# Performance work log

Hardware: AMD Instinct MI355X
Metric: run time of the kernel (lower is better)

The kernel has to match this reference:

```python
import jax, jax.numpy as jnp
import numpy as np

B, T, D = 4, 2048, 1024
H = 16
DH = D // H

def setup_inputs() -> dict:
    key = jax.random.key(0)
    k1, k2, k3 = jax.random.split(key, 3)
    x = jax.random.normal(k1, (B, T, D), dtype=jnp.float32)
    causal_mask = jnp.tril(jnp.ones((T, T), dtype=bool))[None, None]  # (1,1,T,T)
    Wqkv = jax.random.normal(k2, (D, 3 * D), dtype=jnp.float32) * (1.0 / np.sqrt(D))
    Wout = jax.random.normal(k3, (D, D), dtype=jnp.float32) * (1.0 / np.sqrt(D))
    return {"x": x, "causal_mask": causal_mask, "Wqkv": Wqkv, "Wout": Wout}

def reference(x, causal_mask, Wqkv, Wout):
    Bb, Tt, C = x.shape
    scale = jnp.sqrt(jnp.asarray(DH, dtype=x.dtype))
    qkv = x @ Wqkv                                   # (B,T,3D)
    qkv = qkv.reshape(Bb, Tt, 3, H, DH)
    qkv = jnp.transpose(qkv, (2, 0, 3, 1, 4))        # (3,B,H,T,DH)
    q, k, v = qkv[0], qkv[1], qkv[2]
    attn = jnp.einsum('bhqd,bhkd->bhqk', q, k) / scale
    attn = jnp.where(causal_mask, attn, jnp.asarray(-jnp.inf, dtype=attn.dtype))
    attn = jax.nn.softmax(attn, axis=-1)             # dropout p=0 -> identity
    out = jnp.einsum('bhqk,bhkd->bhqd', attn, v)     # (B,H,T,DH)
    out = jnp.transpose(out, (0, 2, 1, 3)).reshape(Bb, Tt, C)
    return out @ Wout
```

## Files before the change

### kernel.cpp

```cpp
#include <hip/hip_runtime.h>
#include <hip/hip_bf16.h>
#include <math.h>


#define Bb 4
#define Tt 2048
#define Dd 1024
#define Hh 16
#define DH 64
#define Mrows (Bb*Tt)
#define NEGBIG (-1.0e30f)
#define KB64 (Dd/64)
#define CHUNKS 1024
#define TILEU16 8192

typedef unsigned short u16;
typedef __attribute__((ext_vector_type(8))) short bf16x8;
typedef __attribute__((ext_vector_type(4))) float f32x4;
typedef __attribute__((ext_vector_type(4))) unsigned int u32x4;

__device__ __forceinline__ u16 f2bf(float f) {
    union { float f; unsigned int i; } v; v.f = f;
    unsigned int x = v.i;
    return (u16)((x + 0x7fffu + ((x >> 16) & 1u)) >> 16);
}

__device__ __forceinline__ unsigned int cvt_pk_bf16(float lo, float hi) {
    unsigned int r;
    asm("v_cvt_pk_bf16_f32 %0, %1, %2" : "=v"(r) : "v"(lo), "v"(hi));
    return r;
}

__device__ __forceinline__ void perm32swap(unsigned& x, unsigned& y) {
    asm("v_permlane32_swap_b32 %0, %1" : "+v"(x), "+v"(y));
}
__device__ __forceinline__ void perm16swap(unsigned& x, unsigned& y) {
    asm("v_permlane16_swap_b32 %0, %1" : "+v"(x), "+v"(y));
}

__device__ __forceinline__ float exp2_(float x) {
#if __has_builtin(__builtin_amdgcn_exp2f)
    return __builtin_amdgcn_exp2f(x);
#else
    return __expf(x * 0.69314718056f);
#endif
}

typedef __attribute__((address_space(1))) const void glob_cv;
typedef __attribute__((address_space(3))) void lds_v;
__device__ __forceinline__ void gl2lds16(const void* g, void* l) {
    __builtin_amdgcn_global_load_lds((glob_cv*)g, (lds_v*)l, 16, 0, 0);
}

__global__ __launch_bounds__(256) void convert_x_tiled(const float* __restrict__ src,
                                                       u16* __restrict__ dst) {
    const int mb = blockIdx.x >> 4, kb = blockIdx.x & 15;
    const int row = threadIdx.x & 127, half = threadIdx.x >> 7;
    const float* s = src + (size_t)(mb * 128 + row) * Dd + kb * 64 + half * 32;
    u16* base = dst + (size_t)blockIdx.x * TILEU16;
    #pragma unroll
    for (int cq = 0; cq < 4; ++cq) {
        const int kq = half * 4 + cq;
        float4 f0 = *(const float4*)(s + cq * 8);
        float4 f1 = *(const float4*)(s + cq * 8 + 4);
        uint4 o;
        o.x = cvt_pk_bf16(f0.x, f0.y); o.y = cvt_pk_bf16(f0.z, f0.w);
        o.z = cvt_pk_bf16(f1.x, f1.y); o.w = cvt_pk_bf16(f1.z, f1.w);
        *(uint4*)(base + (size_t)(kq * 128 + row) * 8) = o;
    }
}

__global__ __launch_bounds__(256) void convert_w_tiled(const float* __restrict__ W,
                                                       u16* __restrict__ Wt,
                                                       int N) {
    __shared__ u16 t[128][68];
    const int nb = blockIdx.x, kb = blockIdx.y;
    const int k0 = kb * 64, n0 = nb * 128;
    const int k = threadIdx.x >> 2, ng = threadIdx.x & 3;
    const float* s = W + (size_t)(k0 + k) * N + n0 + ng * 32;
    #pragma unroll
    for (int i = 0; i < 8; ++i) {
        float4 f = *(const float4*)(s + i * 4);
        const int n = ng * 32 + i * 4;
        t[n + 0][k] = f2bf(f.x); t[n + 1][k] = f2bf(f.y);
        t[n + 2][k] = f2bf(f.z); t[n + 3][k] = f2bf(f.w);
    }
    __syncthreads();
    u16* base = Wt + (size_t)(nb * KB64 + kb) * TILEU16;
    #pragma unroll
    for (int it = 0; it < 4; ++it) {
        const int c = it * 256 + threadIdx.x;
        const int row = c & 127, kq = c >> 7;
        union { u16 u[8]; uint4 v; } o;
        #pragma unroll
        for (int j = 0; j < 8; ++j) o.u[j] = t[row][kq * 8 + j];
        *(uint4*)(base + (size_t)c * 8) = o.v;
    }
}

template <int MODE>
__global__ __launch_bounds__(256) void gemm_mfma(const u16* __restrict__ At,
                                                 const u16* __restrict__ Bt,
                                                 u16* __restrict__ Qo,
                                                 u16* __restrict__ KT,
                                                 u16* __restrict__ VtT,
                                                 float* __restrict__ Out) {
    __shared__ u16 As[8 * 128 * 8];
    __shared__ u16 Bs[8 * 128 * 8];
    const int tid  = threadIdx.x;
    const int lane = tid & 63, w = tid >> 6;
    const int ml   = lane & 15, q = lane >> 4;
    const int wm   = w >> 1, wn = w & 1;
    const int m0 = blockIdx.y * 128;

    const u16* Abase = At + (size_t)blockIdx.y * KB64 * TILEU16;
    const u16* Bbase = Bt + (size_t)blockIdx.x * KB64 * TILEU16;

    f32x4 acc[4][4];
    #pragma unroll
    for (int i = 0; i < 4; ++i)
        #pragma unroll
        for (int j = 0; j < 4; ++j) acc[i][j] = (f32x4){0.f, 0.f, 0.f, 0.f};

    for (int kb = 0; kb < KB64; ++kb) {
        __syncthreads();
        const u16* Ak = Abase + (size_t)kb * TILEU16;
        const u16* Bk = Bbase + (size_t)kb * TILEU16;
        #pragma unroll
        for (int it = 0; it < 4; ++it) {
            const int c = it * 256 + tid;
            gl2lds16(Ak + (size_t)c * 8, (char*)As + c * 16);
            gl2lds16(Bk + (size_t)c * 8, (char*)Bs + c * 16);
        }
        __syncthreads();

        #pragma unroll
        for (int ks = 0; ks < 2; ++ks) {
            const int kq = ks * 4 + q;
            bf16x8 af[4], bfr[4];
            #pragma unroll
            for (int i = 0; i < 4; ++i)
                af[i] = *(const bf16x8*)((const char*)As +
                        ((kq * 128) + wm * 64 + i * 16 + ml) * 16);
            #pragma unroll
            for (int j = 0; j < 4; ++j)
                bfr[j] = *(const bf16x8*)((const char*)Bs +
                        ((kq * 128) + wn * 64 + j * 16 + ml) * 16);
            #pragma unroll
            for (int i = 0; i < 4; ++i)
                #pragma unroll
                for (int j = 0; j < 4; ++j)
                    acc[i][j] = __builtin_amdgcn_mfma_f32_16x16x32_bf16(
                            bfr[j], af[i], acc[i][j], 0, 0, 0);
        }
    }

    if (MODE == 0) {
        const int s  = (blockIdx.x * 128) >> 10;
        const int h0 = ((blockIdx.x * 128) & 1023) >> 6;
        #pragma unroll
        for (int i = 0; i < 4; ++i) {
            const int m  = m0 + wm * 64 + i * 16 + ml;
            const int bb = m >> 11, t = m & 2047;
            const int bhn = bb * Hh + h0 + wn;
            #pragma unroll
            for (int j = 0; j < 4; ++j) {
                const int dh = j * 16 + q * 4;
                if (s == 2) {
                    u16* vb = VtT + (size_t)(bhn * 16 + (t >> 7)) * TILEU16;
                    #pragma unroll
                    for (int r = 0; r < 4; ++r)
                        vb[(size_t)(((t >> 3) & 15) * 64 + dh + r) * 8 + (t & 7)]
                            = f2bf(acc[i][j][r]);
                } else if (s == 1) {
                    uint2 pk;
                    pk.x = cvt_pk_bf16(acc[i][j][0], acc[i][j][1]);
                    pk.y = cvt_pk_bf16(acc[i][j][2], acc[i][j][3]);
                    *(uint2*)(KT + (size_t)(bhn * 16 + (t >> 7)) * TILEU16 +
                              (size_t)((j * 2 + (q >> 1)) * 128 + (t & 127)) * 8 +
                              (q & 1) * 4) = pk;
                } else {
                    const float sc = 0.125f * 1.44269504089f;
                    uint2 pk;
                    pk.x = cvt_pk_bf16(acc[i][j][0] * sc, acc[i][j][1] * sc);
                    pk.y = cvt_pk_bf16(acc[i][j][2] * sc, acc[i][j][3] * sc);
                    *(uint2*)(Qo + ((size_t)bhn * Tt + t) * DH + dh) = pk;
                }
            }
        }
    } else {
        #pragma unroll
        for (int i = 0; i < 4; ++i) {
            const int m = m0 + wm * 64 + i * 16 + ml;
            #pragma unroll
            for (int j = 0; j < 4; ++j) {
                const int n = blockIdx.x * 128 + wn * 64 + j * 16 + q * 4;
                float4 st = {acc[i][j][0], acc[i][j][1], acc[i][j][2], acc[i][j][3]};
                *(float4*)(Out + (size_t)m * Dd + n) = st;
            }
        }
    }
}

__device__ __forceinline__ void softmax_pack(f32x4 (&st)[8], float& m_i, float& l_i,
                                             f32x4 (&accO)[4], unsigned (&d)[8],
                                             unsigned (&e)[8], int q, int qrow,
                                             bool diag) {
    if (diag) {
        #pragma unroll
        for (int kt = 0; kt < 8; ++kt)
            #pragma unroll
            for (int r = 0; r < 4; ++r)
                if (kt * 16 + q * 4 + r > qrow) st[kt][r] = NEGBIG;
    }
    float mx = NEGBIG;
    #pragma unroll
    for (int kt = 0; kt < 8; ++kt) {
        float a0 = fmaxf(st[kt][0], st[kt][1]);
        float a1 = fmaxf(st[kt][2], st[kt][3]);
        mx = fmaxf(fmaxf(mx, a0), a1);
    }
    mx = fmaxf(mx, __shfl_xor(mx, 16, 64));
    mx = fmaxf(mx, __shfl_xor(mx, 32, 64));

    float nm = m_i;
    if (__any(mx > m_i + 8.f)) {
        nm = fmaxf(m_i, mx);
        const float alpha = exp2_(m_i - nm);
        m_i = nm;
        l_i *= alpha;
        #pragma unroll
        for (int dt = 0; dt < 4; ++dt)
            #pragma unroll
            for (int r = 0; r < 4; ++r) accO[dt][r] *= alpha;
    }

    float rs = 0.f;
    #pragma unroll
    for (int kt = 0; kt < 8; ++kt) {
        const float p0 = exp2_(st[kt][0] - nm);
        const float p1 = exp2_(st[kt][1] - nm);
        const float p2 = exp2_(st[kt][2] - nm);
        const float p3 = exp2_(st[kt][3] - nm);
        rs += (p0 + p1) + (p2 + p3);
        d[kt] = cvt_pk_bf16(p0, p1);
        e[kt] = cvt_pk_bf16(p2, p3);
    }
    rs += __shfl_xor(rs, 16, 64);
    rs += __shfl_xor(rs, 32, 64);
    l_i += rs;
}

__device__ __forceinline__ bf16x8 build_bp(const unsigned (&d)[8],
                                           const unsigned (&e)[8], int s) {
    unsigned w0 = d[2 * s], w2 = d[2 * s + 1];
    perm32swap(w0, w2); perm16swap(w0, w2);
    unsigned w1 = e[2 * s], w3 = e[2 * s + 1];
    perm32swap(w1, w3); perm16swap(w1, w3);
    union { u32x4 u; bf16x8 b; } cv;
    cv.u = (u32x4){w0, w1, w2, w3};
    return cv.b;
}

__global__ __launch_bounds__(256, 3) void attn_mfma(const u16* __restrict__ Q,
                                                    const u16* __restrict__ KT,
                                                    const u16* __restrict__ VtT,
                                                    u16* __restrict__ AOT) {
    __shared__ u16 Ks[8 * 128 * 8];
    __shared__ u16 Vs[2][16 * 64 * 8];

    const int tid  = threadIdx.x;
    const int lane = tid & 63, w = tid >> 6;
    const int nl   = lane & 15, q = lane >> 4;
    const int bh = blockIdx.y, b = bh >> 4, h = bh & 15;
    const size_t kbase = (size_t)bh * Tt * DH;

    for (int phase = 0; phase < 2; ++phase) {
        const int qt = phase ? (15 - (int)blockIdx.x) : (int)blockIdx.x;
        const int q0 = qt * 128;
        const int nj = qt + 1;

        bf16x8 qf[2][2];
        #pragma unroll
        for (int qb = 0; qb < 2; ++qb)
            #pragma unroll
            for (int s = 0; s < 2; ++s)
                qf[qb][s] = *(const bf16x8*)(Q + kbase +
                        (size_t)(q0 + w * 32 + qb * 16 + nl) * DH + (s * 4 + q) * 8);

        float m_i[2] = {NEGBIG, NEGBIG};
        float l_i[2] = {0.f, 0.f};
        f32x4 accO[2][4];
        #pragma unroll
        for (int qb = 0; qb < 2; ++qb)
            #pragma unroll
            for (int dt = 0; dt < 4; ++dt) accO[qb][dt] = (f32x4){0.f, 0.f, 0.f, 0.f};

        __syncthreads();
        {
            const u16* Kb = KT  + (size_t)(bh * 16) * TILEU16;
            const u16* Vb = VtT + (size_t)(bh * 16) * TILEU16;
            #pragma unroll
            for (int it = 0; it < 4; ++it) {
                const int c = it * 256 + tid;
                gl2lds16(Kb + (size_t)c * 8, (char*)Ks + c * 16);
                gl2lds16(Vb + (size_t)c * 8, (char*)Vs[0] + c * 16);
            }
        }

        for (int jt = 0; jt < nj; ++jt) {
            const int buf = jt & 1;
            __syncthreads();

            f32x4 st0[8], st1[8];
            #pragma unroll
            for (int kt = 0; kt < 8; ++kt) {
                st0[kt] = (f32x4){0.f, 0.f, 0.f, 0.f};
                st1[kt] = (f32x4){0.f, 0.f, 0.f, 0.f};
            }
            __builtin_amdgcn_s_setprio(1);
            #pragma unroll
            for (int s = 0; s < 2; ++s) {
                #pragma unroll
                for (int kt = 0; kt < 8; ++kt) {
                    bf16x8 ak = *(const bf16x8*)((const char*)Ks +
                            ((s * 4 + q) * 128 + kt * 16 + nl) * 16);
                    st0[kt] = __builtin_amdgcn_mfma_f32_16x16x32_bf16(
                            ak, qf[0][s], st0[kt], 0, 0, 0);
                    st1[kt] = __builtin_amdgcn_mfma_f32_16x16x32_bf16(
                            ak, qf[1][s], st1[kt], 0, 0, 0);
                }
            }
            __builtin_amdgcn_s_setprio(0);

            __syncthreads();

            if (jt + 1 < nj) {
                const u16* Kb = KT  + (size_t)(bh * 16 + jt + 1) * TILEU16;
                const u16* Vb = VtT + (size_t)(bh * 16 + jt + 1) * TILEU16;
                #pragma unroll
                for (int it = 0; it < 4; ++it) {
                    const int c = it * 256 + tid;
                    gl2lds16(Kb + (size_t)c * 8, (char*)Ks + c * 16);
                    gl2lds16(Vb + (size_t)c * 8, (char*)Vs[buf ^ 1] + c * 16);
                }
            }

            const bool diag = (jt == nj - 1);
            unsigned d0[8], e0[8], d1[8], e1[8];
            softmax_pack(st0, m_i[0], l_i[0], accO[0], d0, e0, q, w * 32 + nl, diag);
            softmax_pack(st1, m_i[1], l_i[1], accO[1], d1, e1, q, w * 32 + 16 + nl, diag);

            __builtin_amdgcn_s_setprio(1);
            #pragma unroll
            for (int s = 0; s < 4; ++s) {
                bf16x8 bp0 = build_bp(d0, e0, s);
                bf16x8 bp1 = build_bp(d1, e1, s);
                #pragma unroll
                for (int dt = 0; dt < 4; ++dt) {
                    bf16x8 av = *(const bf16x8*)((const char*)Vs[buf] +
                            ((s * 4 + q) * 64 + dt * 16 + nl) * 16);
                    accO[0][dt] = __builtin_amdgcn_mfma_f32_16x16x32_bf16(
                            av, bp0, accO[0][dt], 0, 0, 0);
                    accO[1][dt] = __builtin_amdgcn_mfma_f32_16x16x32_bf16(
                            av, bp1, accO[1][dt], 0, 0, 0);
                }
            }
            __builtin_amdgcn_s_setprio(0);
        }

        #pragma unroll
        for (int qb = 0; qb < 2; ++qb) {
            const float inv = 1.0f / l_i[qb];
            const int t = q0 + w * 32 + qb * 16 + nl;
            const int m = b * Tt + t;
            u16* ab = AOT + (size_t)((m >> 7) * KB64 + h) * TILEU16;
            #pragma unroll
            for (int dt = 0; dt < 4; ++dt) {
                uint2 pk;
                pk.x = cvt_pk_bf16(accO[qb][dt][0] * inv, accO[qb][dt][1] * inv);
                pk.y = cvt_pk_bf16(accO[qb][dt][2] * inv, accO[qb][dt][3] * inv);
                *(uint2*)(ab + (size_t)((dt * 2 + (q >> 1)) * 128 + (m & 127)) * 8 +
                          (q & 1) * 4) = pk;
            }
        }
    }
}

extern "C" void kernel_launch(void* const* d_in, const int* in_sizes, int n_in,
                              void* d_out, int out_size, void* d_ws, size_t ws_size,
                              hipStream_t stream) {
    const float* x_raw    = (const float*)d_in[0];
    const float* Wqkv_raw = (const float*)d_in[2];
    const float* Wout_raw = (const float*)d_in[3];
    float* out = (float*)d_out;

    const size_t SZ = (size_t)Bb * Hh * Tt * DH;
    u16* ws = (u16*)d_ws;
    u16* Qw     = ws;
    u16* KT     = ws + SZ;
    u16* VtT    = ws + 2 * SZ;
    u16* AOT    = ws + 3 * SZ;
    u16* WqkvT  = ws + 4 * SZ;
    u16* WoutT  = WqkvT + (size_t)3 * Dd * Dd;
    u16* xT     = (u16*)d_out;

    convert_x_tiled<<<dim3(64 * KB64), 256, 0, stream>>>(x_raw, xT);
    convert_w_tiled<<<dim3(3 * Dd / 128, KB64), 256, 0, stream>>>(Wqkv_raw, WqkvT, 3 * Dd);
    convert_w_tiled<<<dim3(Dd / 128, KB64),     256, 0, stream>>>(Wout_raw, WoutT, Dd);

    gemm_mfma<0><<<dim3(3 * Dd / 128, Mrows / 128), 256, 0, stream>>>(xT, WqkvT, Qw, KT, VtT, nullptr);
    attn_mfma  <<<dim3(Tt / 256, Bb * Hh), 256, 0, stream>>>(Qw, KT, VtT, AOT);
    gemm_mfma<1><<<dim3(Dd / 128, Mrows / 128), 256, 0, stream>>>(AOT, WoutT, nullptr, nullptr, nullptr, out);
}
```

Baseline: 273.6 us.

## Fuse conversion kernels and read K/V fragments directly from global memory in attention

Merges the three fp32-to-bf16 conversion launches into one kernel that dispatches on block index, which removes two launches. The attention kernel also drops its LDS double-buffered K/V staging and the barriers around it, and loads MFMA operand fragments straight from global memory (relying on L1/L2), with launch bounds relaxed to allow more occupancy. This trades the synchronisation and LDS traffic for possibly higher global load latency and repeated loads of the same K/V tiles by each wave.

```diff
diff --git a/kernel.cpp b/kernel.cpp
--- a/kernel.cpp
+++ b/kernel.cpp
@@ -52,31 +52,12 @@
     __builtin_amdgcn_global_load_lds((glob_cv*)g, (lds_v*)l, 16, 0, 0);
 }
 
-__global__ __launch_bounds__(256) void convert_x_tiled(const float* __restrict__ src,
-                                                       u16* __restrict__ dst) {
-    const int mb = blockIdx.x >> 4, kb = blockIdx.x & 15;
-    const int row = threadIdx.x & 127, half = threadIdx.x >> 7;
-    const float* s = src + (size_t)(mb * 128 + row) * Dd + kb * 64 + half * 32;
-    u16* base = dst + (size_t)blockIdx.x * TILEU16;
-    #pragma unroll
-    for (int cq = 0; cq < 4; ++cq) {
-        const int kq = half * 4 + cq;
-        float4 f0 = *(const float4*)(s + cq * 8);
-        float4 f1 = *(const float4*)(s + cq * 8 + 4);
-        uint4 o;
-        o.x = cvt_pk_bf16(f0.x, f0.y); o.y = cvt_pk_bf16(f0.z, f0.w);
-        o.z = cvt_pk_bf16(f1.x, f1.y); o.w = cvt_pk_bf16(f1.z, f1.w);
-        *(uint4*)(base + (size_t)(kq * 128 + row) * 8) = o;
-    }
-}
-
-__global__ __launch_bounds__(256) void convert_w_tiled(const float* __restrict__ W,
-                                                       u16* __restrict__ Wt,
-                                                       int N) {
-    __shared__ u16 t[128][68];
-    const int nb = blockIdx.x, kb = blockIdx.y;
+__device__ __forceinline__ void conv_w_body(const float* __restrict__ W,
+                                            u16* __restrict__ Wt, int N,
+                                            int nb, int kb, int tid,
+                                            u16 (*t)[68]) {
     const int k0 = kb * 64, n0 = nb * 128;
-    const int k = threadIdx.x >> 2, ng = threadIdx.x & 3;
+    const int k = tid >> 2, ng = tid & 3;
     const float* s = W + (size_t)(k0 + k) * N + n0 + ng * 32;
     #pragma unroll
     for (int i = 0; i < 8; ++i) {
@@ -89,12 +70,44 @@
     u16* base = Wt + (size_t)(nb * KB64 + kb) * TILEU16;
     #pragma unroll
     for (int it = 0; it < 4; ++it) {
-        const int c = it * 256 + threadIdx.x;
+        const int c = it * 256 + tid;
         const int row = c & 127, kq = c >> 7;
         union { u16 u[8]; uint4 v; } o;
         #pragma unroll
         for (int j = 0; j < 8; ++j) o.u[j] = t[row][kq * 8 + j];
         *(uint4*)(base + (size_t)c * 8) = o.v;
+    }
+}
+
+__global__ __launch_bounds__(256) void convert_all(const float* __restrict__ x,
+                                                   const float* __restrict__ Wqkv,
+                                                   const float* __restrict__ Wout,
+                                                   u16* __restrict__ xT,
+                                                   u16* __restrict__ WqkvT,
+                                                   u16* __restrict__ WoutT) {
+    __shared__ u16 t[128][68];
+    const int bid = blockIdx.x, tid = threadIdx.x;
+    if (bid < 1024) {
+        const int mb = bid >> 4, kb = bid & 15;
+        const int row = tid & 127, half = tid >> 7;
+        const float* s = x + (size_t)(mb * 128 + row) * Dd + kb * 64 + half * 32;
+        u16* base = xT + (size_t)bid * TILEU16;
+        #pragma unroll
+        for (int cq = 0; cq < 4; ++cq) {
+            const int kq = half * 4 + cq;
+            float4 f0 = *(const float4*)(s + cq * 8);
+            float4 f1 = *(const float4*)(s + cq * 8 + 4);
+            uint4 o;
+            o.x = cvt_pk_bf16(f0.x, f0.y); o.y = cvt_pk_bf16(f0.z, f0.w);
+            o.z = cvt_pk_bf16(f1.x, f1.y); o.w = cvt_pk_bf16(f1.z, f1.w);
+            *(uint4*)(base + (size_t)(kq * 128 + row) * 8) = o;
+        }
+    } else if (bid < 1408) {
+        const int r = bid - 1024;
+        conv_w_body(Wqkv, WqkvT, 3 * Dd, r % 24, r / 24, tid, t);
+    } else {
+        const int r = bid - 1408;
+        conv_w_body(Wout, WoutT, Dd, r % 8, r / 8, tid, t);
     }
 }
 
@@ -262,13 +275,10 @@
     return cv.b;
 }
 
-__global__ __launch_bounds__(256, 3) void attn_mfma(const u16* __restrict__ Q,
-                                                    const u16* __restrict__ KT,
-                                                    const u16* __restrict__ VtT,
-                                                    u16* __restrict__ AOT) {
-    __shared__ u16 Ks[8 * 128 * 8];
-    __shared__ u16 Vs[2][16 * 64 * 8];
-
+__global__ __launch_bounds__(256) void attn_mfma(const u16* __restrict__ Q,
+                                                 const u16* __restrict__ KT,
+                                                 const u16* __restrict__ VtT,
+                                                 u16* __restrict__ AOT) {
     const int tid  = threadIdx.x;
     const int lane = tid & 63, w = tid >> 6;
     const int nl   = lane & 15, q = lane >> 4;
@@ -296,22 +306,10 @@
             #pragma unroll
             for (int dt = 0; dt < 4; ++dt) accO[qb][dt] = (f32x4){0.f, 0.f, 0.f, 0.f};
 
-        __syncthreads();
-        {
-            const u16* Kb = KT  + (size_t)(bh * 16) * TILEU16;
-            const u16* Vb = VtT + (size_t)(bh * 16) * TILEU16;
-            #pragma unroll
-            for (int it = 0; it < 4; ++it) {
-                const int c = it * 256 + tid;
-                gl2lds16(Kb + (size_t)c * 8, (char*)Ks + c * 16);
-                gl2lds16(Vb + (size_t)c * 8, (char*)Vs[0] + c * 16);
-            }
-        }
-
-        for (int jt = 0; jt < nj; ++jt) {
-            const int buf = jt & 1;
-            __syncthreads();
-
+        const u16* Kb = KT  + (size_t)(bh * 16) * TILEU16;
+        const u16* Vb = VtT + (size_t)(bh * 16) * TILEU16;
+
+        for (int jt = 0; jt < nj; ++jt, Kb += TILEU16, Vb += TILEU16) {
             f32x4 st0[8], st1[8];
             #pragma unroll
             for (int kt = 0; kt < 8; ++kt) {
@@ -323,8 +321,8 @@
             for (int s = 0; s < 2; ++s) {
                 #pragma unroll
                 for (int kt = 0; kt < 8; ++kt) {
-                    bf16x8 ak = *(const bf16x8*)((const char*)Ks +
-                            ((s * 4 + q) * 128 + kt * 16 + nl) * 16);
+                    bf16x8 ak = *(const bf16x8*)(Kb +
+                            (size_t)(((s * 4 + q) * 128 + kt * 16 + nl) * 8));
                     st0[kt] = __builtin_amdgcn_mfma_f32_16x16x32_bf16(
                             ak, qf[0][s], st0[kt], 0, 0, 0);
                     st1[kt] = __builtin_amdgcn_mfma_f32_16x16x32_bf16(
@@ -333,19 +331,6 @@
             }
             __builtin_amdgcn_s_setprio(0);
 
-            __syncthreads();
-
-            if (jt + 1 < nj) {
-                const u16* Kb = KT  + (size_t)(bh * 16 + jt + 1) * TILEU16;
-                const u16* Vb = VtT + (size_t)(bh * 16 + jt + 1) * TILEU16;
-                #pragma unroll
-                for (int it = 0; it < 4; ++it) {
-                    const int c = it * 256 + tid;
-                    gl2lds16(Kb + (size_t)c * 8, (char*)Ks + c * 16);
-                    gl2lds16(Vb + (size_t)c * 8, (char*)Vs[buf ^ 1] + c * 16);
-                }
-            }
-
             const bool diag = (jt == nj - 1);
             unsigned d0[8], e0[8], d1[8], e1[8];
             softmax_pack(st0, m_i[0], l_i[0], accO[0], d0, e0, q, w * 32 + nl, diag);
@@ -358,8 +343,8 @@
                 bf16x8 bp1 = build_bp(d1, e1, s);
                 #pragma unroll
                 for (int dt = 0; dt < 4; ++dt) {
-                    bf16x8 av = *(const bf16x8*)((const char*)Vs[buf] +
-                            ((s * 4 + q) * 64 + dt * 16 + nl) * 16);
+                    bf16x8 av = *(const bf16x8*)(Vb +
+                            (size_t)(((s * 4 + q) * 64 + dt * 16 + nl) * 8));
                     accO[0][dt] = __builtin_amdgcn_mfma_f32_16x16x32_bf16(
                             av, bp0, accO[0][dt], 0, 0, 0);
                     accO[1][dt] = __builtin_amdgcn_mfma_f32_16x16x32_bf16(
@@ -405,10 +390,8 @@
     u16* WoutT  = WqkvT + (size_t)3 * Dd * Dd;
     u16* xT     = (u16*)d_out;
 
-    convert_x_tiled<<<dim3(64 * KB64), 256, 0, stream>>>(x_raw, xT);
-    convert_w_tiled<<<dim3(3 * Dd / 128, KB64), 256, 0, stream>>>(Wqkv_raw, WqkvT, 3 * Dd);
-    convert_w_tiled<<<dim3(Dd / 128, KB64),     256, 0, stream>>>(Wout_raw, WoutT, Dd);
-
+    convert_all<<<dim3(1536), 256, 0, stream>>>(x_raw, Wqkv_raw, Wout_raw,
+                                                xT, WqkvT, WoutT);
     gemm_mfma<0><<<dim3(3 * Dd / 128, Mrows / 128), 256, 0, stream>>>(xT, WqkvT, Qw, KT, VtT, nullptr);
     attn_mfma  <<<dim3(Tt / 256, Bb * Hh), 256, 0, stream>>>(Qw, KT, VtT, AOT);
     gemm_mfma<1><<<dim3(Dd / 128, Mrows / 128), 256, 0, stream>>>(AOT, WoutT, nullptr, nullptr, nullptr, out);
```

Result: slower. 305.3 us (+11.6%).
